# Kernel tuning notes

Hardware: AMD Instinct MI355X
Metric: run time of the kernel (lower is better)

## Reference

```python
import jax, jax.numpy as jnp
import numpy as np

EPS = 1e-5

def _layernorm(x, w, b):
    # x: [B, L, C]; WithBias_LayerNorm over last dim (biased variance)
    mu = jnp.mean(x, axis=-1, keepdims=True)
    var = jnp.mean((x - mu) ** 2, axis=-1, keepdims=True)
    return (x - mu) / jnp.sqrt(var + EPS) * w + b

def _selective_scan(x, x_proj_w, dt_w, A_logs, Ds):
    # x: [B, D, L]  (D = ssm d_inner = 192, N = d_state = 16, R = dt_rank = 6)
    Bsz, D, L = x.shape
    N = A_logs.shape[1]
    R = dt_w.shape[1]
    x_dbl = jnp.einsum('bdl,rd->blr', x, x_proj_w)            # [B, L, R+2N]
    dts_r = x_dbl[..., :R]
    Bs = x_dbl[..., R:R + N]                                   # [B, L, N]
    Cs = x_dbl[..., R + N:]                                    # [B, L, N]
    dts = jax.nn.softplus(jnp.einsum('blr,dr->bld', dts_r, dt_w))  # [B, L, D]
    As = -jnp.exp(A_logs.astype(jnp.float32))                  # [D, N]
    dt_A = jnp.exp(jnp.einsum('bld,dn->bldn', dts, As))        # [B, L, D, N]
    dt_B_x = jnp.einsum('bld,bln,bdl->bldn', dts, Bs, x)       # [B, L, D, N]

    def step(u, inp):
        a, bx, c = inp                                         # [B,D,N],[B,D,N],[B,N]
        u = a * u + bx
        y = jnp.einsum('bdn,bn->bd', u, c)
        return u, y

    u0 = jnp.zeros((Bsz, D, N), dtype=jnp.float32)
    _, ys = jax.lax.scan(step, u0, (jnp.swapaxes(dt_A, 0, 1),
                                     jnp.swapaxes(dt_B_x, 0, 1),
                                     jnp.swapaxes(Cs, 0, 1)))
    y = jnp.swapaxes(ys, 0, 1)                                 # [B, L, D]
    y = y + jnp.einsum('bdl,d->bld', x, Ds.astype(jnp.float32))
    return y


def setup_inputs() -> dict:
    key = jax.random.key(0)
    ks = jax.random.split(key, 12)
    B, C, H, W = 64, 2048, 24, 8
    D_in2, Dssm, N, R = 384, 192, 16, 6
    s = 0.02
    return {
        'feat_map': jax.random.normal(ks[0], (B, C, H, W), jnp.float32),
        'ln_w': jnp.ones((C,), jnp.float32),
        'ln_b': jnp.zeros((C,), jnp.float32),
        'in_w': jax.random.normal(ks[1], (D_in2, C), jnp.float32) * s,
        'in_b': jnp.zeros((D_in2,), jnp.float32),
        'x_proj_w': jax.random.normal(ks[2], (R + 2 * N, Dssm), jnp.float32) * s,
        'dt_w': jax.random.normal(ks[3], (Dssm, R), jnp.float32) * 0.1,
        'A_logs': jnp.log(jnp.broadcast_to(jnp.arange(1, N + 1, dtype=jnp.float32), (Dssm, N))),
        'Ds': jnp.ones((Dssm,), jnp.float32),
        'out_w': jax.random.normal(ks[4], (C, Dssm), jnp.float32) * s,
        'out_b': jnp.zeros((C,), jnp.float32),
        'mo_w': jax.random.normal(ks[5], (C, C), jnp.float32) * s,
        'mo_b': jnp.zeros((C,), jnp.float32),
        'bn_w': jnp.ones((C,), jnp.float32),
        'bn_b': jnp.zeros((C,), jnp.float32),
        'bn_rm': jax.random.normal(ks[6], (C,), jnp.float32) * 0.1,
        'bn_rv': jax.random.uniform(ks[7], (C,), jnp.float32) + 0.5,
    }


def reference(feat_map, ln_w, ln_b, in_w, in_b, x_proj_w, dt_w, A_logs, Ds,
              out_w, out_b, mo_w, mo_b, bn_w, bn_b, bn_rm, bn_rv):
    B, C, H, W = feat_map.shape
    L = H * W
    x3 = feat_map.transpose(0, 2, 3, 1).reshape(B, L, C)       # to_3d
    fm = _layernorm(x3, ln_w, ln_b)                            # normalized feat_map [B, L, C]
    xz = jnp.einsum('blc,oc->blo', fm, in_w) + in_b            # 1x1 conv in_proj
    x, z = jnp.split(xz, 2, axis=-1)                           # each [B, L, 192]
    xd = jnp.swapaxes(x, 1, 2)                                 # [B, D, L]
    yf = _selective_scan(xd, x_proj_w, dt_w, A_logs, Ds)       # [B, L, D]
    yb = _selective_scan(xd[:, :, ::-1], x_proj_w, dt_w, A_logs, Ds)[:, ::-1, :]
    ssm = yf + yb                                              # [B, L, D]
    ssm = ssm * jax.nn.silu(z)
    out = jnp.einsum('bld,cd->blc', ssm, out_w) + out_b        # out_proj 1x1 conv
    out = out + fm                                             # drop_path is identity at eval
    out = jnp.einsum('blc,oc->blo', out, mo_w) + mo_b          # mamba_out conv 1x1
    out = (out - bn_rm) / jnp.sqrt(bn_rv + EPS) * bn_w + bn_b  # BatchNorm (eval)
    out = jax.nn.relu(out)
    return out.reshape(B, H, W, C).transpose(0, 3, 1, 2)
```

## Files before the change

kernel.cpp:

```cpp
#include <hip/hip_runtime.h>
#include <math.h>

#define EPSV 1e-5f


typedef __attribute__((ext_vector_type(8))) __bf16 bf16x8;
typedef __attribute__((ext_vector_type(4))) float f32x4;

__device__ __forceinline__ ushort f2bf(float f) {
  union { float f; unsigned u; } v; v.f = f;
  const unsigned r = v.u + 0x7fffu + ((v.u >> 16) & 1u);
  return (ushort)(r >> 16);
}

#define GLOAD16(G, L) __builtin_amdgcn_global_load_lds( \
    (__attribute__((address_space(1))) void*)(G), \
    (__attribute__((address_space(3))) void*)(L), 16, 0, 0)

#define BAR() do { asm volatile("" ::: "memory"); \
  __builtin_amdgcn_s_barrier(); \
  asm volatile("" ::: "memory"); } while (0)

__global__ __launch_bounds__(256) void cvt_kernel(
    const float* __restrict__ s, ushort* __restrict__ d, int n)
{
  const int i = (blockIdx.x * 256 + threadIdx.x) * 4;
  if (i + 3 < n) {
    const float4 v = *(const float4*)(s + i);
    ushort4 o;
    o.x = f2bf(v.x); o.y = f2bf(v.y); o.z = f2bf(v.z); o.w = f2bf(v.w);
    *(ushort4*)(d + i) = o;
  }
}

__global__ __launch_bounds__(256) void transpose_w(
    const float* __restrict__ w, ushort* __restrict__ wT)
{
  __shared__ float t[64][65];
  const int c0 = blockIdx.x * 64, d0 = blockIdx.y * 64;
  const int tl = threadIdx.x & 63, tg = threadIdx.x >> 6;
#pragma unroll
  for (int r = 0; r < 16; ++r) {
    const int c = r * 4 + tg;
    t[c][tl] = w[(size_t)(c0 + c) * 192 + d0 + tl];
  }
  __syncthreads();
#pragma unroll
  for (int r = 0; r < 16; ++r) {
    const int d = r * 4 + tg;
    wT[(size_t)(d0 + d) * 2048 + c0 + tl] = f2bf(t[tl][d]);
  }
}

__global__ __launch_bounds__(256) void ln_stats(
    const float* __restrict__ feat, float* __restrict__ sums)
{
  const int b = blockIdx.x, c0 = blockIdx.y * 128;
  const int l = threadIdx.x;
  if (l >= 192) return;
  const float* p = feat + ((size_t)b * 2048 + c0) * 192 + l;
  float s = 0.f, sq = 0.f;
  for (int c = 0; c < 128; ++c) { const float v = p[(size_t)c * 192]; s += v; sq = fmaf(v, v, sq); }
  atomicAdd(&sums[(b * 192 + l) * 2], s);
  atomicAdd(&sums[(b * 192 + l) * 2 + 1], sq);
}

__global__ __launch_bounds__(256) void ln_apply(
    const float* __restrict__ feat, const float* __restrict__ sums,
    const float* __restrict__ lnw, const float* __restrict__ lnb,
    ushort* __restrict__ fm)
{
  __shared__ float tile[64][65];
  __shared__ float smu[64], srs[64];
  const int b = blockIdx.x, c0 = blockIdx.y * 64, l0 = blockIdx.z * 64;
  const int tl = threadIdx.x & 63, tg = threadIdx.x >> 6;
#pragma unroll
  for (int r = 0; r < 16; ++r) {
    const int c = r * 4 + tg;
    tile[c][tl] = feat[((size_t)b * 2048 + c0 + c) * 192 + l0 + tl];
  }
  if (threadIdx.x < 64) {
    const float s  = sums[(b * 192 + l0 + threadIdx.x) * 2];
    const float sq = sums[(b * 192 + l0 + threadIdx.x) * 2 + 1];
    const float mu = s * (1.f / 2048.f);
    smu[threadIdx.x] = mu;
    srs[threadIdx.x] = rsqrtf(sq * (1.f / 2048.f) - mu * mu + EPSV);
  }
  __syncthreads();
  const float w = lnw[c0 + tl], bb = lnb[c0 + tl];
#pragma unroll
  for (int r = 0; r < 16; ++r) {
    const int ll = r * 4 + tg;
    fm[((size_t)(b * 192 + l0 + ll)) * 2048 + c0 + tl] =
        f2bf((tile[tl][ll] - smu[ll]) * srs[ll] * w + bb);
  }
}

__device__ __forceinline__ void mfma_phase(
    const ushort* __restrict__ Ag, int lda,
    const ushort* __restrict__ Bg, int ldb, int K,
    int bm, int bn, int tid, ushort* As, ushort* Bs, f32x4 acc[4][4])
{
  const int lane = tid & 63, wave = tid >> 6;
  const int wm = (wave & 1) << 6, wn = (wave >> 1) << 6;
  const int fr = lane & 15, q = lane >> 4;
  const int r0 = tid >> 2, kc = (tid & 3) << 3;
  const int lb = (tid & 192) * 8;
  for (int k0 = 0; k0 < K; k0 += 32) {
    __syncthreads();
    GLOAD16(Ag + (size_t)(bm + r0) * lda + k0 + kc,      As + lb);
    GLOAD16(Ag + (size_t)(bm + 64 + r0) * lda + k0 + kc, As + 2048 + lb);
    GLOAD16(Bg + (size_t)(bn + r0) * ldb + k0 + kc,      Bs + lb);
    GLOAD16(Bg + (size_t)(bn + 64 + r0) * ldb + k0 + kc, Bs + 2048 + lb);
    __syncthreads();
    bf16x8 af[4], bfr[4];
#pragma unroll
    for (int i = 0; i < 4; ++i) {
      af[i]  = *(const bf16x8*)&As[(wm + i * 16 + fr) * 32 + q * 8];
      bfr[i] = *(const bf16x8*)&Bs[(wn + i * 16 + fr) * 32 + q * 8];
    }
#pragma unroll
    for (int i = 0; i < 4; ++i)
#pragma unroll
      for (int j = 0; j < 4; ++j)
        acc[i][j] = __builtin_amdgcn_mfma_f32_16x16x32_bf16(af[i], bfr[j], acc[i][j], 0, 0, 0);
  }
}

template<int MODE>
__global__ __launch_bounds__(256) void mfma_gemm(
    const ushort* __restrict__ A1, const ushort* __restrict__ B1,
    const float* __restrict__ p0,
    float* __restrict__ out, ushort* __restrict__ outb)
{
  __shared__ ushort As[4096], Bs[4096];
  const int tid = threadIdx.x;
  const int bm = blockIdx.y * 128, bn = blockIdx.x * 128;
  f32x4 acc[4][4];
#pragma unroll
  for (int i = 0; i < 4; ++i)
#pragma unroll
    for (int j = 0; j < 4; ++j) acc[i][j] = (f32x4)(0.f);

  mfma_phase(A1, 2048, B1, 2048, 2048, bm, bn, tid, As, Bs, acc);

  const int lane = tid & 63, wave = tid >> 6;
  const int wm = (wave & 1) << 6, wn = (wave >> 1) << 6;
  const int fr = lane & 15, q = lane >> 4;
  if (MODE == 0) {
#pragma unroll
    for (int mi = 0; mi < 4; ++mi) {
      const int m0 = bm + wm + mi * 16 + q * 4;
#pragma unroll
      for (int ni = 0; ni < 4; ++ni) {
        const int n = bn + wn + ni * 16 + fr;
        const float bias = p0[n];
#pragma unroll
        for (int r = 0; r < 4; ++r)
          out[(size_t)(m0 + r) * 384 + n] = acc[mi][ni][r] + bias;
      }
    }
  } else {
#pragma unroll
    for (int mi = 0; mi < 4; ++mi) {
      const int m0 = bm + wm + mi * 16 + q * 4;
#pragma unroll
      for (int ni = 0; ni < 4; ++ni) {
        const int n = bn + wn + ni * 16 + fr;
#pragma unroll
        for (int r = 0; r < 4; ++r)
          outb[(size_t)(m0 + r) * 256 + n] = f2bf(acc[mi][ni][r]);
      }
    }
  }
}


__device__ __forceinline__ void stage_half(
    int t, int kind,
    int bm, int bn, int tid,
    const ushort* __restrict__ fmw, const ushort* __restrict__ mow,
    const ushort* __restrict__ ssmb, const ushort* __restrict__ w2b,
    ushort* As, ushort* Bs)
{
  const bool isA = (kind < 2);
  const ushort* G; int ld, k0;
  if (t < 32) { G = isA ? fmw : mow;  ld = 2048; k0 = t * 64; }
  else        { G = isA ? ssmb : w2b; ld = 256;  k0 = (t - 32) * 64; }
  const int p0 = isA ? bm : bn;
  ushort* L = (isA ? As : Bs) + (t & 1) * 16384 + (kind & 1) * 8192;
  const int w = tid >> 6, l = tid & 63;
#pragma unroll
  for (int j = 0; j < 2; ++j) {
    const int LC = j * 512 + w * 64 + l;
    const int row = (kind & 1) * 128 + (LC >> 3);
    const int sc = (LC & 7) ^ (row & 7);
    GLOAD16(G + (size_t)(p0 + row) * ld + k0 + sc * 8, L + j * 4096 + w * 512);
  }
}

__global__ __launch_bounds__(512, 2) void mfma_gemm_big(
    const ushort* __restrict__ fmw,  const ushort* __restrict__ mow,
    const ushort* __restrict__ ssmb, const ushort* __restrict__ w2b,
    const float* __restrict__ scale, const float* __restrict__ shift,
    float* __restrict__ out)
{
  __shared__ ushort As[2 * 16384];
  __shared__ ushort Bs[2 * 16384];
  const int tid = threadIdx.x;
  const int flat = blockIdx.x;
  const int bx = flat & 7, by = flat >> 3;
  const int bm = by * 256, bn = bx * 256;

  const int lane = tid & 63, wave = tid >> 6;
  const int wr = wave >> 2, wc = wave & 3;
  const int fr = lane & 15, q = lane >> 4;

  constexpr int NT = 36;

  f32x4 acc[8][4];
#pragma unroll
  for (int i = 0; i < 8; ++i)
#pragma unroll
    for (int j = 0; j < 4; ++j) acc[i][j] = (f32x4)(0.f);

  stage_half(0, 0, bm, bn, tid, fmw, mow, ssmb, w2b, As, Bs);
  stage_half(0, 1, bm, bn, tid, fmw, mow, ssmb, w2b, As, Bs);
  stage_half(0, 2, bm, bn, tid, fmw, mow, ssmb, w2b, As, Bs);
  stage_half(0, 3, bm, bn, tid, fmw, mow, ssmb, w2b, As, Bs);
  stage_half(1, 2, bm, bn, tid, fmw, mow, ssmb, w2b, As, Bs);
  stage_half(1, 3, bm, bn, tid, fmw, mow, ssmb, w2b, As, Bs);
  asm volatile("s_waitcnt vmcnt(4)" ::: "memory");
  BAR();

  for (int t = 0; t < NT; ++t) {
    const ushort* Ab = As + (t & 1) * 16384;
    const ushort* Bb = Bs + (t & 1) * 16384;
    bf16x8 bfr[4];
#pragma unroll
    for (int ph = 0; ph < 4; ++ph) {
      const int ks = ph >> 1, mh = ph & 1;
      const int kswz = (((ks << 2) + q) ^ (fr & 7)) << 3;
      bf16x8 af[4];
#pragma unroll
      for (int mi = 0; mi < 4; ++mi)
        af[mi] = *(const bf16x8*)&Ab[(wr * 128 + mh * 64 + mi * 16 + fr) * 64 + kswz];
      if (mh == 0) {
#pragma unroll
        for (int ni = 0; ni < 4; ++ni)
          bfr[ni] = *(const bf16x8*)&Bb[(wc * 64 + ni * 16 + fr) * 64 + kswz];
      }
      if (ph == 0) {
        if (t + 1 < NT) stage_half(t + 1, 0, bm, bn, tid, fmw, mow, ssmb, w2b, As, Bs);
      } else if (ph == 1) {
        if (t + 1 < NT) stage_half(t + 1, 1, bm, bn, tid, fmw, mow, ssmb, w2b, As, Bs);
      } else if (ph == 3) {
        if (t + 2 < NT) {
          stage_half(t + 2, 2, bm, bn, tid, fmw, mow, ssmb, w2b, As, Bs);
          stage_half(t + 2, 3, bm, bn, tid, fmw, mow, ssmb, w2b, As, Bs);
        }
      }
      BAR();
      __builtin_amdgcn_s_setprio(1);
#pragma unroll
      for (int mi = 0; mi < 4; ++mi)
#pragma unroll
        for (int ni = 0; ni < 4; ++ni)
          acc[mh * 4 + mi][ni] = __builtin_amdgcn_mfma_f32_16x16x32_bf16(
              af[mi], bfr[ni], acc[mh * 4 + mi][ni], 0, 0, 0);
      __builtin_amdgcn_s_setprio(0);
      if (ph == 3) {
        if (t <= 33) asm volatile("s_waitcnt vmcnt(4)" ::: "memory");
        else if (t == 34) asm volatile("s_waitcnt vmcnt(0)" ::: "memory");
      }
      BAR();
    }
  }

#pragma unroll
  for (int mi = 0; mi < 8; ++mi) {
    const int m0 = bm + wr * 128 + mi * 16 + q * 4;
    const int b = m0 / 192, l0 = m0 - b * 192;
#pragma unroll
    for (int ni = 0; ni < 4; ++ni) {
      const int n = bn + wc * 64 + ni * 16 + fr;
      const float sc = scale[n], sh = shift[n];
      float4 o;
      o.x = fmaxf(fmaf(acc[mi][ni][0], sc, sh), 0.f);
      o.y = fmaxf(fmaf(acc[mi][ni][1], sc, sh), 0.f);
      o.z = fmaxf(fmaf(acc[mi][ni][2], sc, sh), 0.f);
      o.w = fmaxf(fmaf(acc[mi][ni][3], sc, sh), 0.f);
      *(float4*)(out + ((size_t)b * 2048 + n) * 192 + l0) = o;
    }
  }
}

__global__ __launch_bounds__(64) void xproj_kernel(
    const float* __restrict__ xz, const float* __restrict__ xpw,
    const float* __restrict__ dtw, float* __restrict__ dts,
    float* __restrict__ Bsb, float* __restrict__ Csb)
{
  const int m = blockIdx.x, tid = threadIdx.x;
  __shared__ float xrow[192];
  __shared__ float xdbl[38];
  const float* src = xz + (size_t)m * 384;
#pragma unroll
  for (int i = 0; i < 3; ++i) xrow[tid + i * 64] = src[tid + i * 64];
  __syncthreads();
  if (tid < 38) {
    float a = 0.f;
    const float* wr = xpw + tid * 192;
    for (int d = 0; d < 192; ++d) a = fmaf(xrow[d], wr[d], a);
    xdbl[tid] = a;
  }
  __syncthreads();
  if (tid < 16) Bsb[(size_t)m * 16 + tid] = xdbl[6 + tid];
  else if (tid < 32) Csb[(size_t)m * 16 + (tid - 16)] = xdbl[22 + (tid - 16)];
#pragma unroll
  for (int i = 0; i < 3; ++i) {
    const int d = tid + i * 64;
    const float* w = dtw + d * 6;
    float a = xdbl[0] * w[0] + xdbl[1] * w[1] + xdbl[2] * w[2]
            + xdbl[3] * w[3] + xdbl[4] * w[4] + xdbl[5] * w[5];
    dts[(size_t)m * 192 + d] = (a > 20.f) ? a : log1pf(__expf(a));
  }
}

__global__ __launch_bounds__(256) void scan_kernel(
    const float* __restrict__ xz, const float* __restrict__ dts,
    const float* __restrict__ Bsb, const float* __restrict__ Csb,
    const float* __restrict__ A_logs, const float* __restrict__ Ds,
    ushort* __restrict__ ssm)
{
  __shared__ float s_dt[3072], s_x[3072], s_B[3072], s_C[3072], s_y[3072];
  const int tid = threadIdx.x;
  const int b = blockIdx.x / 12, dblk = blockIdx.x - b * 12;
  const int d0 = dblk * 16;
  const size_t rbase = (size_t)b * 192;
  for (int i = tid; i < 768; i += 256) {
    const int l = i >> 2, j = (i & 3) << 2;
    const size_t row = rbase + l;
    ((float4*)s_dt)[i] = *(const float4*)(dts + row * 192 + d0 + j);
    ((float4*)s_x)[i]  = *(const float4*)(xz  + row * 384 + d0 + j);
    ((float4*)s_B)[i]  = *(const float4*)(Bsb + row * 16 + j);
    ((float4*)s_C)[i]  = *(const float4*)(Csb + row * 16 + j);
  }
  __syncthreads();
  const int n = tid & 15, dl = tid >> 4;
  const float Acoef = -expf(A_logs[(d0 + dl) * 16 + n]);
  float u = 0.f;
#pragma unroll 4
  for (int l = 0; l < 192; ++l) {
    const float dt = s_dt[l * 16 + dl];
    const float c  = dt * s_B[l * 16 + n] * s_x[l * 16 + dl];
    const float a  = __expf(dt * Acoef);
    u = fmaf(a, u, c);
    float y = u * s_C[l * 16 + n];
    y += __shfl_xor(y, 1, 16); y += __shfl_xor(y, 2, 16);
    y += __shfl_xor(y, 4, 16); y += __shfl_xor(y, 8, 16);
    if (n == 0) s_y[l * 16 + dl] = y;
  }
  u = 0.f;
#pragma unroll 4
  for (int l = 191; l >= 0; --l) {
    const float dt = s_dt[l * 16 + dl];
    const float c  = dt * s_B[l * 16 + n] * s_x[l * 16 + dl];
    const float a  = __expf(dt * Acoef);
    u = fmaf(a, u, c);
    float y = u * s_C[l * 16 + n];
    y += __shfl_xor(y, 1, 16); y += __shfl_xor(y, 2, 16);
    y += __shfl_xor(y, 4, 16); y += __shfl_xor(y, 8, 16);
    if (n == 0) s_y[l * 16 + dl] += y;
  }
  __syncthreads();
  for (int i = tid; i < 768; i += 256) {
    const int l = i >> 2, j = (i & 3) << 2;
    const size_t row = rbase + l;
    const float4 y4 = ((const float4*)s_y)[i];
    const float4 x4 = ((const float4*)s_x)[i];
    const float4 z4 = *(const float4*)(xz + row * 384 + 192 + d0 + j);
    const float4 D4 = *(const float4*)(Ds + d0 + j);
    ushort4 o;
    o.x = f2bf((y4.x + 2.f * x4.x * D4.x) * (z4.x / (1.f + __expf(-z4.x))));
    o.y = f2bf((y4.y + 2.f * x4.y * D4.y) * (z4.y / (1.f + __expf(-z4.y))));
    o.z = f2bf((y4.z + 2.f * x4.z * D4.z) * (z4.z / (1.f + __expf(-z4.z))));
    o.w = f2bf((y4.w + 2.f * x4.w * D4.w) * (z4.w / (1.f + __expf(-z4.w))));
    *(ushort4*)(ssm + row * 256 + d0 + j) = o;
  }
}

__global__ __launch_bounds__(64) void prep_kernel(
    const float* __restrict__ mo_w, const float* __restrict__ mo_b,
    const float* __restrict__ out_b,
    const float* __restrict__ bn_w, const float* __restrict__ bn_b,
    const float* __restrict__ bn_rm, const float* __restrict__ bn_rv,
    float* __restrict__ scale, float* __restrict__ shift)
{
  const int o = blockIdx.x, tid = threadIdx.x;
  float s = 0.f;
  for (int c = tid; c < 2048; c += 64) s = fmaf(mo_w[(size_t)o * 2048 + c], out_b[c], s);
#pragma unroll
  for (int off = 32; off > 0; off >>= 1) s += __shfl_down(s, off, 64);
  if (tid == 0) {
    const float b2 = s + mo_b[o];
    const float sc = bn_w[o] * rsqrtf(bn_rv[o] + EPSV);
    scale[o] = sc;
    shift[o] = (b2 - bn_rm[o]) * sc + bn_b[o];
  }
}

extern "C" void kernel_launch(void* const* d_in, const int* in_sizes, int n_in,
                              void* d_out, int out_size, void* d_ws, size_t ws_size,
                              hipStream_t stream) {
  const float* feat  = (const float*)d_in[0];
  const float* ln_w  = (const float*)d_in[1];
  const float* ln_b  = (const float*)d_in[2];
  const float* in_w  = (const float*)d_in[3];
  const float* in_b  = (const float*)d_in[4];
  const float* xpw   = (const float*)d_in[5];
  const float* dtw   = (const float*)d_in[6];
  const float* A_logs= (const float*)d_in[7];
  const float* Ds    = (const float*)d_in[8];
  const float* out_w = (const float*)d_in[9];
  const float* out_b = (const float*)d_in[10];
  const float* mo_w  = (const float*)d_in[11];
  const float* mo_b  = (const float*)d_in[12];
  const float* bn_w  = (const float*)d_in[13];
  const float* bn_b  = (const float*)d_in[14];
  const float* bn_rm = (const float*)d_in[15];
  const float* bn_rv = (const float*)d_in[16];
  float* out = (float*)d_out;

  uint8_t* p = (uint8_t*)d_ws;
  ushort* fm_b  = (ushort*)p; p += (size_t)12288 * 2048 * 2;
  float*  xz    = (float*)p;  p += (size_t)12288 * 384 * 4;
  float*  dts   = (float*)p;  p += (size_t)12288 * 192 * 4;
  float*  Bsb   = (float*)p;  p += (size_t)12288 * 16 * 4;
  float*  Csb   = (float*)p;  p += (size_t)12288 * 16 * 4;
  ushort* ssm_b = (ushort*)p; p += (size_t)12288 * 256 * 2;
  ushort* W2b   = (ushort*)p; p += (size_t)2048 * 256 * 2;
  ushort* owT_b = (ushort*)p; p += (size_t)256 * 2048 * 2;
  ushort* mo_wb = (ushort*)p; p += (size_t)2048 * 2048 * 2;
  ushort* in_wb = (ushort*)p; p += (size_t)384 * 2048 * 2;
  float*  scale = (float*)p;  p += 2048 * 4;
  float*  shift = (float*)p;  p += 2048 * 4;
  float*  sums  = (float*)p;  p += (size_t)64 * 192 * 2 * 4;
  if ((size_t)(p - (uint8_t*)d_ws) > ws_size) return;

  cvt_kernel<<<4096, 256, 0, stream>>>(mo_w, mo_wb, 2048 * 2048);
  cvt_kernel<<<768, 256, 0, stream>>>(in_w, in_wb, 384 * 2048);
  hipMemsetAsync(owT_b, 0, (size_t)256 * 2048 * 2, stream);
  hipMemsetAsync(ssm_b, 0, (size_t)12288 * 256 * 2, stream);
  transpose_w<<<dim3(32, 3), 256, 0, stream>>>(out_w, owT_b);

  hipMemsetAsync(sums, 0, (size_t)64 * 192 * 2 * 4, stream);
  ln_stats<<<dim3(64, 16), 256, 0, stream>>>(feat, sums);
  ln_apply<<<dim3(64, 32, 3), 256, 0, stream>>>(feat, sums, ln_w, ln_b, fm_b);

  mfma_gemm<0><<<dim3(3, 96), 256, 0, stream>>>(
      fm_b, in_wb, in_b, xz, nullptr);

  xproj_kernel<<<12288, 64, 0, stream>>>(xz, xpw, dtw, dts, Bsb, Csb);
  scan_kernel<<<768, 256, 0, stream>>>(xz, dts, Bsb, Csb, A_logs, Ds, ssm_b);

  mfma_gemm<2><<<dim3(2, 16), 256, 0, stream>>>(
      mo_wb, owT_b, nullptr, nullptr, W2b);
  prep_kernel<<<2048, 64, 0, stream>>>(mo_w, mo_b, out_b, bn_w, bn_b, bn_rm, bn_rv, scale, shift);

  mfma_gemm_big<<<384, 512, 0, stream>>>(fm_b, mo_wb, ssm_b, W2b, scale, shift, out);
}
```

Baseline: 701.2 us.

## Transpose scan shared-memory layout and use DPP row reductions in selective scan

```diff
diff --git a/kernel.cpp b/kernel.cpp
--- a/kernel.cpp
+++ b/kernel.cpp
@@ -20,6 +20,19 @@
 #define BAR() do { asm volatile("" ::: "memory"); \
   __builtin_amdgcn_s_barrier(); \
   asm volatile("" ::: "memory"); } while (0)
+
+template<int CTRL>
+__device__ __forceinline__ float dpp_add(float y) {
+  const int s = __builtin_amdgcn_update_dpp(0, __float_as_int(y), CTRL, 0xF, 0xF, true);
+  return y + __int_as_float(s);
+}
+__device__ __forceinline__ float reduce16(float y) {
+  y = dpp_add<0xB1>(y);
+  y = dpp_add<0x4E>(y);
+  y = dpp_add<0x124>(y);
+  y = dpp_add<0x128>(y);
+  return y;
+}
 
 __global__ __launch_bounds__(256) void cvt_kernel(
     const float* __restrict__ s, ushort* __restrict__ d, int n)
@@ -174,7 +187,6 @@
     }
   }
 }
-
 
 __device__ __forceinline__ void stage_half(
     int t, int kind,
@@ -332,7 +344,8 @@
     const float* __restrict__ A_logs, const float* __restrict__ Ds,
     ushort* __restrict__ ssm)
 {
-  __shared__ float s_dt[3072], s_x[3072], s_B[3072], s_C[3072], s_y[3072];
+  __shared__ float s_dt[16 * 196], s_x[16 * 196], s_B[16 * 196],
+                   s_C[16 * 196], s_y[16 * 196];
   const int tid = threadIdx.x;
   const int b = blockIdx.x / 12, dblk = blockIdx.x - b * 12;
   const int d0 = dblk * 16;
@@ -340,44 +353,66 @@
   for (int i = tid; i < 768; i += 256) {
     const int l = i >> 2, j = (i & 3) << 2;
     const size_t row = rbase + l;
-    ((float4*)s_dt)[i] = *(const float4*)(dts + row * 192 + d0 + j);
-    ((float4*)s_x)[i]  = *(const float4*)(xz  + row * 384 + d0 + j);
-    ((float4*)s_B)[i]  = *(const float4*)(Bsb + row * 16 + j);
-    ((float4*)s_C)[i]  = *(const float4*)(Csb + row * 16 + j);
+    const float4 dtv = *(const float4*)(dts + row * 192 + d0 + j);
+    const float4 xv  = *(const float4*)(xz  + row * 384 + d0 + j);
+    const float4 Bv  = *(const float4*)(Bsb + row * 16 + j);
+    const float4 Cv  = *(const float4*)(Csb + row * 16 + j);
+    s_dt[(j + 0) * 196 + l] = dtv.x; s_dt[(j + 1) * 196 + l] = dtv.y;
+    s_dt[(j + 2) * 196 + l] = dtv.z; s_dt[(j + 3) * 196 + l] = dtv.w;
+    s_x [(j + 0) * 196 + l] = xv.x;  s_x [(j + 1) * 196 + l] = xv.y;
+    s_x [(j + 2) * 196 + l] = xv.z;  s_x [(j + 3) * 196 + l] = xv.w;
+    s_B [(j + 0) * 196 + l] = Bv.x;  s_B [(j + 1) * 196 + l] = Bv.y;
+    s_B [(j + 2) * 196 + l] = Bv.z;  s_B [(j + 3) * 196 + l] = Bv.w;
+    s_C [(j + 0) * 196 + l] = Cv.x;  s_C [(j + 1) * 196 + l] = Cv.y;
+    s_C [(j + 2) * 196 + l] = Cv.z;  s_C [(j + 3) * 196 + l] = Cv.w;
   }
   __syncthreads();
   const int n = tid & 15, dl = tid >> 4;
   const float Acoef = -expf(A_logs[(d0 + dl) * 16 + n]);
+  const float* pdt = s_dt + dl * 196;
+  const float* px  = s_x  + dl * 196;
+  const float* pB  = s_B  + n * 196;
+  const float* pC  = s_C  + n * 196;
+  float* py = s_y + dl * 196;
   float u = 0.f;
-#pragma unroll 4
-  for (int l = 0; l < 192; ++l) {
-    const float dt = s_dt[l * 16 + dl];
-    const float c  = dt * s_B[l * 16 + n] * s_x[l * 16 + dl];
-    const float a  = __expf(dt * Acoef);
-    u = fmaf(a, u, c);
-    float y = u * s_C[l * 16 + n];
-    y += __shfl_xor(y, 1, 16); y += __shfl_xor(y, 2, 16);
-    y += __shfl_xor(y, 4, 16); y += __shfl_xor(y, 8, 16);
-    if (n == 0) s_y[l * 16 + dl] = y;
+  for (int l0 = 0; l0 < 192; l0 += 4) {
+    const float4 dtv = *(const float4*)(pdt + l0);
+    const float4 xv  = *(const float4*)(px + l0);
+    const float4 Bv  = *(const float4*)(pB + l0);
+    const float4 Cv  = *(const float4*)(pC + l0);
+    u = fmaf(__expf(dtv.x * Acoef), u, dtv.x * Bv.x * xv.x);
+    { float y = reduce16(u * Cv.x); if (n == 0) py[l0 + 0] = y; }
+    u = fmaf(__expf(dtv.y * Acoef), u, dtv.y * Bv.y * xv.y);
+    { float y = reduce16(u * Cv.y); if (n == 0) py[l0 + 1] = y; }
+    u = fmaf(__expf(dtv.z * Acoef), u, dtv.z * Bv.z * xv.z);
+    { float y = reduce16(u * Cv.z); if (n == 0) py[l0 + 2] = y; }
+    u = fmaf(__expf(dtv.w * Acoef), u, dtv.w * Bv.w * xv.w);
+    { float y = reduce16(u * Cv.w); if (n == 0) py[l0 + 3] = y; }
   }
   u = 0.f;
-#pragma unroll 4
-  for (int l = 191; l >= 0; --l) {
-    const float dt = s_dt[l * 16 + dl];
-    const float c  = dt * s_B[l * 16 + n] * s_x[l * 16 + dl];
-    const float a  = __expf(dt * Acoef);
-    u = fmaf(a, u, c);
-    float y = u * s_C[l * 16 + n];
-    y += __shfl_xor(y, 1, 16); y += __shfl_xor(y, 2, 16);
-    y += __shfl_xor(y, 4, 16); y += __shfl_xor(y, 8, 16);
-    if (n == 0) s_y[l * 16 + dl] += y;
+  for (int l0 = 188; l0 >= 0; l0 -= 4) {
+    const float4 dtv = *(const float4*)(pdt + l0);
+    const float4 xv  = *(const float4*)(px + l0);
+    const float4 Bv  = *(const float4*)(pB + l0);
+    const float4 Cv  = *(const float4*)(pC + l0);
+    u = fmaf(__expf(dtv.w * Acoef), u, dtv.w * Bv.w * xv.w);
+    { float y = reduce16(u * Cv.w); if (n == 0) py[l0 + 3] += y; }
+    u = fmaf(__expf(dtv.z * Acoef), u, dtv.z * Bv.z * xv.z);
+    { float y = reduce16(u * Cv.z); if (n == 0) py[l0 + 2] += y; }
+    u = fmaf(__expf(dtv.y * Acoef), u, dtv.y * Bv.y * xv.y);
+    { float y = reduce16(u * Cv.y); if (n == 0) py[l0 + 1] += y; }
+    u = fmaf(__expf(dtv.x * Acoef), u, dtv.x * Bv.x * xv.x);
+    { float y = reduce16(u * Cv.x); if (n == 0) py[l0 + 0] += y; }
   }
   __syncthreads();
   for (int i = tid; i < 768; i += 256) {
     const int l = i >> 2, j = (i & 3) << 2;
     const size_t row = rbase + l;
-    const float4 y4 = ((const float4*)s_y)[i];
-    const float4 x4 = ((const float4*)s_x)[i];
+    float4 y4, x4;
+    y4.x = s_y[(j + 0) * 196 + l]; y4.y = s_y[(j + 1) * 196 + l];
+    y4.z = s_y[(j + 2) * 196 + l]; y4.w = s_y[(j + 3) * 196 + l];
+    x4.x = s_x[(j + 0) * 196 + l]; x4.y = s_x[(j + 1) * 196 + l];
+    x4.z = s_x[(j + 2) * 196 + l]; x4.w = s_x[(j + 3) * 196 + l];
     const float4 z4 = *(const float4*)(xz + row * 384 + 192 + d0 + j);
     const float4 D4 = *(const float4*)(Ds + d0 + j);
     ushort4 o;
```

Result: faster. 608.7 us (-13.2%).
